# Kernel optimization log

Measured on AMD Instinct MI355X. Metric: run time of the kernel, lower is better.

The kernel has to match this reference:

```python
import jax, jax.numpy as jnp
import numpy as np

H, C, D = 8, 32, 128  # num_heads, att_head_size, inp_dim
LN_EPS = 1e-5


def setup_inputs() -> dict:
    key = jax.random.key(0)
    ks = jax.random.split(key, 12)
    B, I, L = 1, 128, 256
    z_ij = jax.random.normal(ks[0], (B, I, L, D), dtype=jnp.float32)
    d_jk = jax.random.uniform(ks[1], (B, L, L, 1), dtype=jnp.float32)
    mask_z = jnp.ones((B, I, L), dtype=jnp.float32)
    s = 0.05
    return {
        "z_ij": z_ij,
        "d_jk": d_jk,
        "mask_z": mask_z,
        "ln_gamma": jnp.ones((D,), jnp.float32),
        "ln_beta": jnp.zeros((D,), jnp.float32),
        "Wq": jax.random.normal(ks[2], (D, H * C), jnp.float32) * s,
        "Wk": jax.random.normal(ks[3], (D, H * C), jnp.float32) * s,
        "Wv": jax.random.normal(ks[4], (D, H * C), jnp.float32) * s,
        "Wb": jax.random.normal(ks[5], (D, H), jnp.float32) * s,
        "Wd": jax.random.normal(ks[6], (1, H), jnp.float32) * s,
        "Wg": jax.random.normal(ks[7], (D, H * C), jnp.float32) * s,
        "bg": jnp.zeros((H * C,), jnp.float32),
        "Wf": jax.random.normal(ks[8], (H * C, D), jnp.float32) * s,
        "bf": jnp.zeros((D,), jnp.float32),
    }


def reference(z_ij, d_jk, mask_z, ln_gamma, ln_beta, Wq, Wk, Wv, Wb, Wd, Wg, bg, Wf, bf):
    B, I, L, _ = z_ij.shape
    # LayerNorm over last dim
    mu = jnp.mean(z_ij, axis=-1, keepdims=True)
    var = jnp.mean(jnp.square(z_ij - mu), axis=-1, keepdims=True)
    z = (z_ij - mu) * jax.lax.rsqrt(var + LN_EPS) * ln_gamma + ln_beta

    rs = lambda x: x.reshape(x.shape[:-1] + (H, C))  # [..., H*C] -> [..., H, C]
    q = rs(z @ Wq) * (H ** -0.5)                  # [B,I,L,H,C]
    k = rs(z @ Wk)                                # [B,I,L,H,C]
    v = rs(z @ Wv)                                # [B,I,L,H,C]

    b = jnp.transpose(z @ Wb, (0, 1, 3, 2))[..., None]       # [B,I,H,Q,1]
    d = jnp.transpose(d_jk @ Wd, (0, 3, 1, 2))[:, None]      # [B,1,H,Q,K]

    logits = jnp.einsum('biqhc,bikhc->bihqk', q, k) + b + d  # [B,I,H,Q,K]
    att_mask = 1e9 * (mask_z[:, :, None, None, :] - 1.0)
    logits = logits + att_mask
    weights = jax.nn.softmax(logits, axis=-1)

    weighted = jnp.einsum('bihqk,bikhc->biqhc', weights, v)  # [B,I,Q,H,C]
    g = jax.nn.sigmoid(rs(z @ Wg + bg))                      # [B,I,Q,H,C]
    out = (g * weighted).reshape(B, I, L, H * C)
    out = out @ Wf + bf
    out = out * mask_z[..., None]
    return out
```

## Files before the change

### kernel.cpp

```cpp
#include <hip/hip_runtime.h>
#include <hip/hip_bf16.h>
#include <math.h>

#define HH 8
#define CC 32
#define DD 128
#define HC 256
#define II 128
#define LL 256
#define NROW (II*LL)
#define LN_EPS 1e-5f

typedef float f32x4 __attribute__((ext_vector_type(4)));
typedef short short8 __attribute__((ext_vector_type(8)));
typedef short short4v __attribute__((ext_vector_type(4)));
typedef unsigned short us;

static __device__ __forceinline__ us bfc(float x) {
    return __builtin_bit_cast(us, __float2bfloat16(x));
}
static __device__ __forceinline__ float bf2f(us h) {
    return __builtin_bit_cast(float, ((unsigned int)h) << 16);
}

__global__ __launch_bounds__(256) void k_ln(const float* __restrict__ z,
                                            const float* __restrict__ gamma,
                                            const float* __restrict__ beta,
                                            us* __restrict__ zn)
{
    const int t = threadIdx.x;
    const int row = blockIdx.x * 4 + (t >> 6);
    const int lane = t & 63;
    float2 x = *(const float2*)(z + (size_t)row * DD + lane * 2);
    float s = x.x + x.y;
    float s2 = x.x * x.x + x.y * x.y;
#pragma unroll
    for (int off = 1; off < 64; off <<= 1) {
        s  += __shfl_xor(s, off, 64);
        s2 += __shfl_xor(s2, off, 64);
    }
    float mu = s * (1.0f / DD);
    float var = s2 * (1.0f / DD) - mu * mu;
    float rstd = rsqrtf(var + LN_EPS);
    float2 gm = *(const float2*)(gamma + lane * 2);
    float2 bt = *(const float2*)(beta + lane * 2);
    float y0 = (x.x - mu) * rstd * gm.x + bt.x;
    float y1 = (x.y - mu) * rstd * gm.y + bt.y;
    unsigned int pk = (unsigned int)bfc(y0) | ((unsigned int)bfc(y1) << 16);
    ((unsigned int*)zn)[(size_t)row * 64 + lane] = pk;
}

__global__ __launch_bounds__(256) void k_wprep(const float* __restrict__ Wq,
                                               const float* __restrict__ Wk,
                                               const float* __restrict__ Wv,
                                               const float* __restrict__ Wg,
                                               const float* __restrict__ Wf,
                                               us* __restrict__ F,
                                               us* __restrict__ WfpH,
                                               us* __restrict__ WfpL)
{
    const int bid = blockIdx.x;
    if (bid < 128) {
        const int mat = bid >> 5;
        const float* W = (mat == 0) ? Wq : (mat == 1) ? Wk : (mat == 2) ? Wv : Wg;
        const float scale = (mat == 0) ? 0.35355339059327373f : 1.0f;
        int base = (bid & 31) * 1024 + threadIdx.x * 4;
        float4 wv = *(const float4*)(W + base);
        int k = base >> 8, n0 = base & 255;
        int ks = k >> 5, kk = k & 31;
        int slot = ((kk >> 4) << 2) | (kk & 3);
        int gg = (kk >> 2) & 3;
        float vals[4] = {wv.x, wv.y, wv.z, wv.w};
        us* Fb = F + mat * 32768;
#pragma unroll
        for (int e = 0; e < 4; ++e) {
            int n = n0 + e;
            int lane = (n & 15) | (gg << 4);
            Fb[((size_t)(ks * 16 + (n >> 4)) * 64 + lane) * 8 + slot] = bfc(vals[e] * scale);
        }
    } else {
        int idx = ((bid - 128) * 256 + threadIdx.x) * 4;
#pragma unroll
        for (int e = 0; e < 4; ++e, ++idx) {
            int k = idx >> 7, n = idx & 127;
            float w = Wf[idx];
            us hi = bfc(w);
            us lo = bfc(w - bf2f(hi));
            int kk = k & 31;
            int g = (kk >> 2) & 3, b = kk >> 4, j0 = kk & 3;
            int lane = (n & 15) | (g << 4);
            size_t dst = ((size_t)((k >> 5) * 8 + (n >> 4)) * 64 + lane) * 8 + b * 4 + j0;
            WfpH[dst] = hi;
            WfpL[dst] = lo;
        }
    }
}

__global__ __launch_bounds__(256, 4) void k_proj(const us* __restrict__ zn,
                                                 const us* __restrict__ F,
                                                 const float* __restrict__ bg,
                                                 us* __restrict__ P)
{
    const int rb = blockIdx.x, cb = blockIdx.y, t = threadIdx.x;
    const int m0 = rb * 128, n0 = cb * 128;
    const int mat = n0 >> 8, lc0 = n0 & 255;
    __shared__ us A[128][136];

#pragma unroll
    for (int e = 0; e < 8; ++e) {
        int cid = e * 256 + t;
        int row = cid >> 4, c = cid & 15;
        uint4 q = *(const uint4*)(zn + (size_t)(m0 + row) * DD + c * 8);
        int ks = c >> 2, cc = c & 3;
        int fe = (cc & 1) * 16 + (cc >> 1) * 4;
        *(uint2*)&A[row][ks * 32 + fe]     = make_uint2(q.x, q.y);
        *(uint2*)&A[row][ks * 32 + fe + 8] = make_uint2(q.z, q.w);
    }
    __syncthreads();

    const int lane = t & 63, w = t >> 6;
    const int wm = w & 1, wn = w >> 1;
    const int l0 = lane & 15, g = lane >> 4;
    const us* Fb = F + mat * 32768 + ((size_t)((lc0 >> 4) + wn * 4) * 64 + lane) * 8;
    f32x4 acc[4][4];
#pragma unroll
    for (int a = 0; a < 4; ++a)
#pragma unroll
        for (int b = 0; b < 4; ++b) acc[a][b] = (f32x4){0, 0, 0, 0};

#pragma unroll
    for (int ks = 0; ks < 4; ++ks) {
        short8 af[4], bfr[4];
#pragma unroll
        for (int mf = 0; mf < 4; ++mf)
            af[mf] = *(const short8*)&A[wm * 64 + mf * 16 + l0][ks * 32 + 8 * g];
#pragma unroll
        for (int nf = 0; nf < 4; ++nf)
            bfr[nf] = *(const short8*)(Fb + (size_t)(ks * 16 + nf) * 512);
#pragma unroll
        for (int mf = 0; mf < 4; ++mf)
#pragma unroll
            for (int nf = 0; nf < 4; ++nf)
                acc[mf][nf] = __builtin_amdgcn_mfma_f32_16x16x32_bf16(af[mf], bfr[nf], acc[mf][nf], 0, 0, 0);
    }

    __syncthreads();
    us (*Cs)[136] = A;
#pragma unroll
    for (int nf = 0; nf < 4; ++nf) {
        int lcol = wn * 64 + nf * 16 + l0;
        float bgv = (mat == 3) ? bg[lc0 + lcol] : 0.0f;
#pragma unroll
        for (int mf = 0; mf < 4; ++mf) {
#pragma unroll
            for (int r = 0; r < 4; ++r) {
                float v = acc[mf][nf][r];
                if (mat == 3) v = 1.0f / (1.0f + __expf(-(v + bgv)));
                Cs[wm * 64 + mf * 16 + 4 * g + r][lcol] = bfc(v);
            }
        }
    }
    __syncthreads();

#pragma unroll
    for (int e = 0; e < 8; ++e) {
        int cid = e * 256 + t;
        int row = cid >> 4, c = cid & 15;
        short8 vv = *(const short8*)&Cs[row][c * 8];
        *(short8*)(P + (size_t)(m0 + row) * 1024 + mat * 256 + lc0 + c * 8) = vv;
    }
}

__global__ __launch_bounds__(256) void k_attn(us* __restrict__ P,
                                              const float* __restrict__ djk,
                                              const float* __restrict__ Wd,
                                              const float* __restrict__ mask)
{
    const int i = blockIdx.x, h = blockIdx.y, t = threadIdx.x;
    const size_t rowbase = (size_t)i * LL * 1024;
    const int hoff = h * CC;
    __shared__ us ksl[LL][40];
    __shared__ us vt[CC][264];
    __shared__ float madd[LL];

#pragma unroll
    for (int e = 0; e < 4; ++e) {
        int cid = e * 256 + t;
        int row = cid >> 2, c = cid & 3;
        uint4 q = *(const uint4*)(P + rowbase + (size_t)row * 1024 + 256 + hoff + c * 8);
        int fe = (c & 1) * 16 + (c >> 1) * 4;
        *(uint2*)&ksl[row][fe]     = make_uint2(q.x, q.y);
        *(uint2*)&ksl[row][fe + 8] = make_uint2(q.z, q.w);
    }
#pragma unroll
    for (int e = 0; e < 4; ++e) {
        int cid = e * 256 + t;
        int r = cid >> 2, c = cid & 3;
        short8 vv = *(const short8*)(P + rowbase + (size_t)r * 1024 + 512 + hoff + c * 8);
        int kk = r & 31;
        int pos = (r >> 5) * 32 + 8 * ((kk & 15) >> 2) + 4 * (kk >> 4) + (kk & 3);
#pragma unroll
        for (int u = 0; u < 8; ++u)
            vt[c * 8 + u][pos] = (us)vv[u];
    }
    madd[t] = 1e9f * (mask[i * LL + t] - 1.0f);

    const int lane = t & 63, w = t >> 6;
    const int l0 = lane & 15, g = lane >> 4;
    const int q0 = w * 64;
    const float wd = Wd[h];

    short8 qf[4];
    const float* djk_q[4];
    int qrow[4];
#pragma unroll
    for (int qt = 0; qt < 4; ++qt) {
        qrow[qt] = q0 + qt * 16 + l0;
        djk_q[qt] = djk + (size_t)qrow[qt] * LL;
        const us* qb = P + rowbase + (size_t)qrow[qt] * 1024 + hoff;
        short4v a = *(const short4v*)(qb + 4 * g);
        short4v b = *(const short4v*)(qb + 16 + 4 * g);
        qf[qt][0] = a.x; qf[qt][1] = a.y; qf[qt][2] = a.z; qf[qt][3] = a.w;
        qf[qt][4] = b.x; qf[qt][5] = b.y; qf[qt][6] = b.z; qf[qt][7] = b.w;
    }
    __syncthreads();

    f32x4 oacc[2][4];
#pragma unroll
    for (int ct = 0; ct < 2; ++ct)
#pragma unroll
        for (int qt = 0; qt < 4; ++qt) oacc[ct][qt] = (f32x4){0, 0, 0, 0};
    float ssum[4] = {0, 0, 0, 0};

    for (int p = 0; p < 8; ++p) {
        us pf[4][2][4];
#pragma unroll
        for (int half = 0; half < 2; ++half) {
            const int kt = 2 * p + half;
            const int krow = kt * 16 + l0;
            short8 kf = *(const short8*)&ksl[krow][8 * g];
            f32x4 mvv = *(const f32x4*)&madd[kt * 16 + 4 * g];
#pragma unroll
            for (int qt = 0; qt < 4; ++qt) {
                f32x4 z4 = {0, 0, 0, 0};
                f32x4 s = __builtin_amdgcn_mfma_f32_16x16x32_bf16(kf, qf[qt], z4, 0, 0, 0);
                f32x4 dv = *(const f32x4*)(djk_q[qt] + kt * 16 + 4 * g);
                float p0 = __expf(s[0] + wd * dv.x + mvv.x);
                float p1 = __expf(s[1] + wd * dv.y + mvv.y);
                float p2 = __expf(s[2] + wd * dv.z + mvv.z);
                float p3 = __expf(s[3] + wd * dv.w + mvv.w);
                ssum[qt] += (p0 + p1) + (p2 + p3);
                pf[qt][half][0] = bfc(p0); pf[qt][half][1] = bfc(p1);
                pf[qt][half][2] = bfc(p2); pf[qt][half][3] = bfc(p3);
            }
        }
#pragma unroll
        for (int ct = 0; ct < 2; ++ct) {
            short8 vf = *(const short8*)&vt[ct * 16 + l0][32 * p + 8 * g];
#pragma unroll
            for (int qt = 0; qt < 4; ++qt) {
                short8 pfr;
#pragma unroll
                for (int j = 0; j < 4; ++j) {
                    pfr[j]     = (short)pf[qt][0][j];
                    pfr[j + 4] = (short)pf[qt][1][j];
                }
                oacc[ct][qt] = __builtin_amdgcn_mfma_f32_16x16x32_bf16(vf, pfr, oacc[ct][qt], 0, 0, 0);
            }
        }
    }

    __syncthreads();
    us (*gs)[40] = (us (*)[40])ksl;
#pragma unroll
    for (int qt = 0; qt < 4; ++qt) {
        float s = ssum[qt];
        s += __shfl_xor(s, 16, 64);
        s += __shfl_xor(s, 32, 64);
        float inv = 1.0f / s;
        const us* base = P + rowbase + (size_t)qrow[qt] * 1024 + hoff;
#pragma unroll
        for (int ct = 0; ct < 2; ++ct) {
            short4v gv = *(const short4v*)(base + 768 + ct * 16 + 4 * g);
            f32x4 ov = oacc[ct][qt];
            short4v res;
            res.x = (short)bfc(bf2f((us)gv.x) * ov.x * inv);
            res.y = (short)bfc(bf2f((us)gv.y) * ov.y * inv);
            res.z = (short)bfc(bf2f((us)gv.z) * ov.z * inv);
            res.w = (short)bfc(bf2f((us)gv.w) * ov.w * inv);
            *(short4v*)&gs[qrow[qt]][ct * 16 + 4 * g] = res;
        }
    }
    __syncthreads();
#pragma unroll
    for (int e = 0; e < 4; ++e) {
        int cid = e * 256 + t;
        int row = cid >> 2, c = cid & 3;
        short8 vv = *(const short8*)&gs[row][c * 8];
        *(short8*)(P + rowbase + (size_t)row * 1024 + hoff + c * 8) = vv;
    }
}

__global__ __launch_bounds__(256) void k_out(const us* __restrict__ P,
                                             const us* __restrict__ WfpH,
                                             const us* __restrict__ WfpL,
                                             const float* __restrict__ bf_,
                                             const float* __restrict__ mask,
                                             float* __restrict__ out)
{
    const int t = threadIdx.x;
    const int m0 = blockIdx.x * 64;
    __shared__ us A[64][264];
#pragma unroll
    for (int e = 0; e < 8; ++e) {
        int cid = e * 256 + t;
        int row = cid >> 5, c = cid & 31;
        uint4 q = *(const uint4*)(P + (size_t)(m0 + row) * 1024 + c * 8);
        int ksb = c >> 2, cc = c & 3;
        int fe = (cc & 1) * 16 + (cc >> 1) * 4;
        *(uint2*)&A[row][ksb * 32 + fe]     = make_uint2(q.x, q.y);
        *(uint2*)&A[row][ksb * 32 + fe + 8] = make_uint2(q.z, q.w);
    }
    __syncthreads();
    const int lane = t & 63, w = t >> 6;
    const int l0 = lane & 15, g = lane >> 4;
    f32x4 acc[8];
#pragma unroll
    for (int nf = 0; nf < 8; ++nf) acc[nf] = (f32x4){0, 0, 0, 0};

#pragma unroll
    for (int ksb = 0; ksb < 8; ++ksb) {
        short8 af = *(const short8*)&A[w * 16 + l0][ksb * 32 + 8 * g];
#pragma unroll
        for (int nf = 0; nf < 8; ++nf) {
            short8 bh = *(const short8*)(WfpH + ((size_t)(ksb * 8 + nf) * 64 + lane) * 8);
            short8 bl = *(const short8*)(WfpL + ((size_t)(ksb * 8 + nf) * 64 + lane) * 8);
            acc[nf] = __builtin_amdgcn_mfma_f32_16x16x32_bf16(af, bh, acc[nf], 0, 0, 0);
            acc[nf] = __builtin_amdgcn_mfma_f32_16x16x32_bf16(af, bl, acc[nf], 0, 0, 0);
        }
    }
    float maskv[4];
    int rowm[4];
#pragma unroll
    for (int r = 0; r < 4; ++r) {
        rowm[r] = m0 + w * 16 + 4 * g + r;
        maskv[r] = mask[rowm[r]];
    }
#pragma unroll
    for (int nf = 0; nf < 8; ++nf) {
        int n = nf * 16 + l0;
        float bfv = bf_[n];
#pragma unroll
        for (int r = 0; r < 4; ++r)
            out[(size_t)rowm[r] * DD + n] = (acc[nf][r] + bfv) * maskv[r];
    }
}

extern "C" void kernel_launch(void* const* d_in, const int* in_sizes, int n_in,
                              void* d_out, int out_size, void* d_ws, size_t ws_size,
                              hipStream_t stream)
{
    const float* z     = (const float*)d_in[0];
    const float* djk   = (const float*)d_in[1];
    const float* mask  = (const float*)d_in[2];
    const float* gamma = (const float*)d_in[3];
    const float* beta  = (const float*)d_in[4];
    const float* Wq    = (const float*)d_in[5];
    const float* Wk    = (const float*)d_in[6];
    const float* Wv    = (const float*)d_in[7];
    const float* Wd    = (const float*)d_in[9];
    const float* Wg    = (const float*)d_in[10];
    const float* bg    = (const float*)d_in[11];
    const float* Wf    = (const float*)d_in[12];
    const float* bf_   = (const float*)d_in[13];
    float* out = (float*)d_out;

    us* zn   = (us*)d_ws;
    us* P    = zn + (size_t)NROW * DD;
    us* WfpH = P + (size_t)NROW * 1024;
    us* WfpL = WfpH + 256 * 128;
    us* F    = WfpL + 256 * 128;

    k_ln   <<<NROW / 4, 256, 0, stream>>>(z, gamma, beta, zn);
    k_wprep<<<160, 256, 0, stream>>>(Wq, Wk, Wv, Wg, Wf, F, WfpH, WfpL);
    k_proj <<<dim3(NROW / 128, 8), 256, 0, stream>>>(zn, F, bg, P);
    k_attn <<<dim3(II, HH), 256, 0, stream>>>(P, djk, Wd, mask);
    k_out  <<<NROW / 64, 256, 0, stream>>>(P, WfpH, WfpL, bf_, mask, out);
}
```

Measured before the change: 107.3 us.

## Write Q/K/V in MFMA fragment layout from projection; split attention over query halves

The projection kernel now writes Q and K directly in per-(i,h) MFMA fragment order and V pre-transposed into fragment order, with gate and attention output kept in separate compact buffers. The attention kernel then loads fragments straight from global memory with no shared-memory staging or transpose, and the grid doubles by splitting each (i,h) into two query halves of 128 rows. This removes LDS staging, the scalar V transpose and a barrier in attention, but K/V fragments are reread from global/L2 by both query-half blocks, and the V transpose moves into k_proj as strided LDS gathers.

```diff
diff --git a/kernel.cpp b/kernel.cpp
--- a/kernel.cpp
+++ b/kernel.cpp
@@ -99,7 +99,10 @@
 __global__ __launch_bounds__(256, 4) void k_proj(const us* __restrict__ zn,
                                                  const us* __restrict__ F,
                                                  const float* __restrict__ bg,
-                                                 us* __restrict__ P)
+                                                 us* __restrict__ Qf,
+                                                 us* __restrict__ Kf,
+                                                 us* __restrict__ Vtf,
+                                                 us* __restrict__ Pg)
 {
     const int rb = blockIdx.x, cb = blockIdx.y, t = threadIdx.x;
     const int m0 = rb * 128, n0 = cb * 128;
@@ -162,146 +165,155 @@
     }
     __syncthreads();
 
-#pragma unroll
-    for (int e = 0; e < 8; ++e) {
-        int cid = e * 256 + t;
-        int row = cid >> 4, c = cid & 15;
-        short8 vv = *(const short8*)&Cs[row][c * 8];
-        *(short8*)(P + (size_t)(m0 + row) * 1024 + mat * 256 + lc0 + c * 8) = vv;
-    }
-}
-
-__global__ __launch_bounds__(256) void k_attn(us* __restrict__ P,
+    const int i = m0 >> 8, half = (m0 >> 7) & 1;
+    if (mat <= 1) {
+        us* Dst = (mat == 0) ? Qf : Kf;
+#pragma unroll
+        for (int e = 0; e < 8; ++e) {
+            int sub = e * 256 + t;
+            int lane2 = sub & 63;
+            int l0b = lane2 & 15, gb = lane2 >> 4;
+            int rest = sub >> 6;
+            int hl = rest & 3, ktl = rest >> 2;
+            int hglob = (lc0 >> 5) + hl;
+            int kt = half * 8 + ktl;
+            short8 vv = *(const short8*)&Cs[ktl * 16 + l0b][hl * 32 + 8 * gb];
+            *(short8*)(Dst + (((size_t)(i * 8 + hglob) * 16 + kt) * 64 + lane2) * 8) = vv;
+        }
+    } else if (mat == 2) {
+#pragma unroll
+        for (int e = 0; e < 8; ++e) {
+            int sub = e * 256 + t;
+            int lane2 = sub & 63;
+            int l0b = lane2 & 15, gb = lane2 >> 4;
+            int rest = sub >> 6;
+            int ct = rest & 1, pl = (rest >> 1) & 3, hl = rest >> 3;
+            int hglob = (lc0 >> 5) + hl;
+            int p = half * 4 + pl;
+            int col = hl * 32 + ct * 16 + l0b;
+            us vals[8];
+#pragma unroll
+            for (int j = 0; j < 8; ++j) {
+                int kk = 4 * gb + (j & 3) + 16 * (j >> 2);
+                vals[j] = Cs[pl * 32 + kk][col];
+            }
+            *(short8*)(Vtf + ((((size_t)(i * 8 + hglob) * 8 + p) * 2 + ct) * 64 + lane2) * 8)
+                = *(short8*)vals;
+        }
+    } else {
+#pragma unroll
+        for (int e = 0; e < 8; ++e) {
+            int cid = e * 256 + t;
+            int row = cid >> 4, c = cid & 15;
+            short8 vv = *(const short8*)&Cs[row][c * 8];
+            *(short8*)(Pg + (size_t)(m0 + row) * 256 + lc0 + c * 8) = vv;
+        }
+    }
+}
+
+__global__ __launch_bounds__(256) void k_attn(const us* __restrict__ Qf,
+                                              const us* __restrict__ Kf,
+                                              const us* __restrict__ Vtf,
+                                              const us* __restrict__ Pg,
+                                              us* __restrict__ Po,
                                               const float* __restrict__ djk,
                                               const float* __restrict__ Wd,
                                               const float* __restrict__ mask)
 {
-    const int i = blockIdx.x, h = blockIdx.y, t = threadIdx.x;
-    const size_t rowbase = (size_t)i * LL * 1024;
-    const int hoff = h * CC;
-    __shared__ us ksl[LL][40];
-    __shared__ us vt[CC][264];
-    __shared__ float madd[LL];
-
-#pragma unroll
-    for (int e = 0; e < 4; ++e) {
-        int cid = e * 256 + t;
-        int row = cid >> 2, c = cid & 3;
-        uint4 q = *(const uint4*)(P + rowbase + (size_t)row * 1024 + 256 + hoff + c * 8);
-        int fe = (c & 1) * 16 + (c >> 1) * 4;
-        *(uint2*)&ksl[row][fe]     = make_uint2(q.x, q.y);
-        *(uint2*)&ksl[row][fe + 8] = make_uint2(q.z, q.w);
-    }
-#pragma unroll
-    for (int e = 0; e < 4; ++e) {
-        int cid = e * 256 + t;
-        int r = cid >> 2, c = cid & 3;
-        short8 vv = *(const short8*)(P + rowbase + (size_t)r * 1024 + 512 + hoff + c * 8);
-        int kk = r & 31;
-        int pos = (r >> 5) * 32 + 8 * ((kk & 15) >> 2) + 4 * (kk >> 4) + (kk & 3);
-#pragma unroll
-        for (int u = 0; u < 8; ++u)
-            vt[c * 8 + u][pos] = (us)vv[u];
-    }
-    madd[t] = 1e9f * (mask[i * LL + t] - 1.0f);
-
+    const int ih = blockIdx.x, qh = blockIdx.y;
+    const int i = ih >> 3, h = ih & 7;
+    const int t = threadIdx.x;
     const int lane = t & 63, w = t >> 6;
     const int l0 = lane & 15, g = lane >> 4;
-    const int q0 = w * 64;
+    const int q0 = qh * 128 + w * 32;
+    __shared__ us gs[128][40];
+
     const float wd = Wd[h];
-
-    short8 qf[4];
-    const float* djk_q[4];
-    int qrow[4];
-#pragma unroll
-    for (int qt = 0; qt < 4; ++qt) {
+    const us* Qb = Qf + (size_t)ih * 8192;
+    const us* Kb = Kf + (size_t)ih * 8192;
+    const us* Vb = Vtf + (size_t)ih * 8192;
+
+    short8 qfr[2];
+    int qrow[2];
+    const float* djkq[2];
+#pragma unroll
+    for (int qt = 0; qt < 2; ++qt) {
+        qfr[qt] = *(const short8*)(Qb + ((size_t)((q0 >> 4) + qt) * 64 + lane) * 8);
         qrow[qt] = q0 + qt * 16 + l0;
-        djk_q[qt] = djk + (size_t)qrow[qt] * LL;
-        const us* qb = P + rowbase + (size_t)qrow[qt] * 1024 + hoff;
-        short4v a = *(const short4v*)(qb + 4 * g);
-        short4v b = *(const short4v*)(qb + 16 + 4 * g);
-        qf[qt][0] = a.x; qf[qt][1] = a.y; qf[qt][2] = a.z; qf[qt][3] = a.w;
-        qf[qt][4] = b.x; qf[qt][5] = b.y; qf[qt][6] = b.z; qf[qt][7] = b.w;
-    }
-    __syncthreads();
-
-    f32x4 oacc[2][4];
+        djkq[qt] = djk + (size_t)qrow[qt] * LL;
+    }
+
+    f32x4 oacc[2][2];
 #pragma unroll
     for (int ct = 0; ct < 2; ++ct)
 #pragma unroll
-        for (int qt = 0; qt < 4; ++qt) oacc[ct][qt] = (f32x4){0, 0, 0, 0};
-    float ssum[4] = {0, 0, 0, 0};
+        for (int qt = 0; qt < 2; ++qt) oacc[ct][qt] = (f32x4){0, 0, 0, 0};
+    float ssum[2] = {0, 0};
 
     for (int p = 0; p < 8; ++p) {
-        us pf[4][2][4];
-#pragma unroll
-        for (int half = 0; half < 2; ++half) {
-            const int kt = 2 * p + half;
-            const int krow = kt * 16 + l0;
-            short8 kf = *(const short8*)&ksl[krow][8 * g];
-            f32x4 mvv = *(const f32x4*)&madd[kt * 16 + 4 * g];
-#pragma unroll
-            for (int qt = 0; qt < 4; ++qt) {
+        short8 pfv[2];
+#pragma unroll
+        for (int hf = 0; hf < 2; ++hf) {
+            const int kt = 2 * p + hf;
+            short8 kfr = *(const short8*)(Kb + ((size_t)kt * 64 + lane) * 8);
+            f32x4 mv = *(const f32x4*)(mask + i * LL + kt * 16 + 4 * g);
+            float ma0 = 1e9f * (mv.x - 1.0f), ma1 = 1e9f * (mv.y - 1.0f);
+            float ma2 = 1e9f * (mv.z - 1.0f), ma3 = 1e9f * (mv.w - 1.0f);
+#pragma unroll
+            for (int qt = 0; qt < 2; ++qt) {
                 f32x4 z4 = {0, 0, 0, 0};
-                f32x4 s = __builtin_amdgcn_mfma_f32_16x16x32_bf16(kf, qf[qt], z4, 0, 0, 0);
-                f32x4 dv = *(const f32x4*)(djk_q[qt] + kt * 16 + 4 * g);
-                float p0 = __expf(s[0] + wd * dv.x + mvv.x);
-                float p1 = __expf(s[1] + wd * dv.y + mvv.y);
-                float p2 = __expf(s[2] + wd * dv.z + mvv.z);
-                float p3 = __expf(s[3] + wd * dv.w + mvv.w);
+                f32x4 s = __builtin_amdgcn_mfma_f32_16x16x32_bf16(kfr, qfr[qt], z4, 0, 0, 0);
+                f32x4 dv = *(const f32x4*)(djkq[qt] + kt * 16 + 4 * g);
+                float p0 = __expf(s[0] + wd * dv.x + ma0);
+                float p1 = __expf(s[1] + wd * dv.y + ma1);
+                float p2 = __expf(s[2] + wd * dv.z + ma2);
+                float p3 = __expf(s[3] + wd * dv.w + ma3);
                 ssum[qt] += (p0 + p1) + (p2 + p3);
-                pf[qt][half][0] = bfc(p0); pf[qt][half][1] = bfc(p1);
-                pf[qt][half][2] = bfc(p2); pf[qt][half][3] = bfc(p3);
+                pfv[qt][hf * 4 + 0] = (short)bfc(p0);
+                pfv[qt][hf * 4 + 1] = (short)bfc(p1);
+                pfv[qt][hf * 4 + 2] = (short)bfc(p2);
+                pfv[qt][hf * 4 + 3] = (short)bfc(p3);
             }
         }
 #pragma unroll
         for (int ct = 0; ct < 2; ++ct) {
-            short8 vf = *(const short8*)&vt[ct * 16 + l0][32 * p + 8 * g];
-#pragma unroll
-            for (int qt = 0; qt < 4; ++qt) {
-                short8 pfr;
-#pragma unroll
-                for (int j = 0; j < 4; ++j) {
-                    pfr[j]     = (short)pf[qt][0][j];
-                    pfr[j + 4] = (short)pf[qt][1][j];
-                }
-                oacc[ct][qt] = __builtin_amdgcn_mfma_f32_16x16x32_bf16(vf, pfr, oacc[ct][qt], 0, 0, 0);
-            }
-        }
-    }
-
-    __syncthreads();
-    us (*gs)[40] = (us (*)[40])ksl;
-#pragma unroll
-    for (int qt = 0; qt < 4; ++qt) {
+            short8 vfr = *(const short8*)(Vb + ((size_t)(p * 2 + ct) * 64 + lane) * 8);
+#pragma unroll
+            for (int qt = 0; qt < 2; ++qt)
+                oacc[ct][qt] = __builtin_amdgcn_mfma_f32_16x16x32_bf16(vfr, pfv[qt], oacc[ct][qt], 0, 0, 0);
+        }
+    }
+
+#pragma unroll
+    for (int qt = 0; qt < 2; ++qt) {
         float s = ssum[qt];
         s += __shfl_xor(s, 16, 64);
         s += __shfl_xor(s, 32, 64);
         float inv = 1.0f / s;
-        const us* base = P + rowbase + (size_t)qrow[qt] * 1024 + hoff;
+        const us* gb = Pg + (size_t)(i * LL + qrow[qt]) * 256 + h * CC;
 #pragma unroll
         for (int ct = 0; ct < 2; ++ct) {
-            short4v gv = *(const short4v*)(base + 768 + ct * 16 + 4 * g);
+            short4v gv = *(const short4v*)(gb + ct * 16 + 4 * g);
             f32x4 ov = oacc[ct][qt];
             short4v res;
             res.x = (short)bfc(bf2f((us)gv.x) * ov.x * inv);
             res.y = (short)bfc(bf2f((us)gv.y) * ov.y * inv);
             res.z = (short)bfc(bf2f((us)gv.z) * ov.z * inv);
             res.w = (short)bfc(bf2f((us)gv.w) * ov.w * inv);
-            *(short4v*)&gs[qrow[qt]][ct * 16 + 4 * g] = res;
+            *(short4v*)&gs[w * 32 + qt * 16 + l0][ct * 16 + 4 * g] = res;
         }
     }
     __syncthreads();
 #pragma unroll
-    for (int e = 0; e < 4; ++e) {
+    for (int e = 0; e < 2; ++e) {
         int cid = e * 256 + t;
         int row = cid >> 2, c = cid & 3;
         short8 vv = *(const short8*)&gs[row][c * 8];
-        *(short8*)(P + rowbase + (size_t)row * 1024 + hoff + c * 8) = vv;
-    }
-}
-
-__global__ __launch_bounds__(256) void k_out(const us* __restrict__ P,
+        *(short8*)(Po + (size_t)(i * LL + qh * 128 + row) * 256 + h * CC + c * 8) = vv;
+    }
+}
+
+__global__ __launch_bounds__(256) void k_out(const us* __restrict__ Po,
                                              const us* __restrict__ WfpH,
                                              const us* __restrict__ WfpL,
                                              const float* __restrict__ bf_,
@@ -315,7 +327,7 @@
     for (int e = 0; e < 8; ++e) {
         int cid = e * 256 + t;
         int row = cid >> 5, c = cid & 31;
-        uint4 q = *(const uint4*)(P + (size_t)(m0 + row) * 1024 + c * 8);
+        uint4 q = *(const uint4*)(Po + (size_t)(m0 + row) * 256 + c * 8);
         int ksb = c >> 2, cc = c & 3;
         int fe = (cc & 1) * 16 + (cc >> 1) * 4;
         *(uint2*)&A[row][ksb * 32 + fe]     = make_uint2(q.x, q.y);
@@ -376,14 +388,18 @@
     float* out = (float*)d_out;
 
     us* zn   = (us*)d_ws;
-    us* P    = zn + (size_t)NROW * DD;
-    us* WfpH = P + (size_t)NROW * 1024;
+    us* Qf   = zn   + (size_t)NROW * DD;
+    us* Kf   = Qf   + (size_t)1024 * 8192;
+    us* Vtf  = Kf   + (size_t)1024 * 8192;
+    us* Pg   = Vtf  + (size_t)1024 * 8192;
+    us* Po   = Pg   + (size_t)NROW * 256;
+    us* WfpH = Po   + (size_t)NROW * 256;
     us* WfpL = WfpH + 256 * 128;
     us* F    = WfpL + 256 * 128;
 
     k_ln   <<<NROW / 4, 256, 0, stream>>>(z, gamma, beta, zn);
     k_wprep<<<160, 256, 0, stream>>>(Wq, Wk, Wv, Wg, Wf, F, WfpH, WfpL);
-    k_proj <<<dim3(NROW / 128, 8), 256, 0, stream>>>(zn, F, bg, P);
-    k_attn <<<dim3(II, HH), 256, 0, stream>>>(P, djk, Wd, mask);
-    k_out  <<<NROW / 64, 256, 0, stream>>>(P, WfpH, WfpL, bf_, mask, out);
-}
+    k_proj <<<dim3(NROW / 128, 8), 256, 0, stream>>>(zn, F, bg, Qf, Kf, Vtf, Pg);
+    k_attn <<<dim3(II * HH, 2), 256, 0, stream>>>(Qf, Kf, Vtf, Pg, Po, djk, Wd, mask);
+    k_out  <<<NROW / 64, 256, 0, stream>>>(Po, WfpH, WfpL, bf_, mask, out);
+}
```

New measurement: 102.4 us. -4.6%, faster.
